# Kernel tuning notes

Measured on AMD Instinct MI355X. Metric: run time of the kernel, lower is better.

The kernel has to match this reference:

```python
import jax, jax.numpy as jnp
import numpy as np

B, VS, VO = 16, 10475, 8192
K, PS, PO = 64, 1024, 2048


def setup_inputs() -> dict:
    key = jax.random.key(0)
    k1, k2, k3, k4, k5 = jax.random.split(key, 5)
    smplx_v = jax.random.normal(k1, (B, VS, 3), dtype=jnp.float32)
    object_v = jax.random.normal(k2, (B, VO, 3), dtype=jnp.float32)
    smpl_part_idx = jax.random.randint(k3, (K, PS), 0, VS, dtype=jnp.int64) if jax.config.jax_enable_x64 else jax.random.randint(k3, (K, PS), 0, VS, dtype=jnp.int32)
    obj_part_idx = jax.random.randint(k4, (K, PO), 0, VO, dtype=jnp.int32)
    batch_idx = jax.random.randint(k5, (K,), 0, B, dtype=jnp.int32)
    return {
        'smplx_v': smplx_v,
        'object_v': object_v,
        'smpl_part_idx': smpl_part_idx,
        'obj_part_idx': obj_part_idx,
        'batch_idx': batch_idx,
    }


def reference(smplx_v, object_v, smpl_part_idx, obj_part_idx, batch_idx):
    # Batched gather of per-pair contact vertex subsets.
    sc = smplx_v[batch_idx[:, None], smpl_part_idx]   # [K, PS, 3]
    oc = object_v[batch_idx[:, None], obj_part_idx]   # [K, PO, 3]
    # Pairwise Euclidean distances [K, PS, PO] (torch.norm of differences).
    diff = sc[:, :, None, :] - oc[:, None, :, :]
    d = jnp.sqrt(jnp.sum(diff * diff, axis=-1))
    # One-directional chamfer: min over object verts, mean over smpl verts,
    # then mean over all contact pairs (torch.stack(...).mean()).
    loss = jnp.mean(jnp.mean(jnp.min(d, axis=-1), axis=-1))
    return loss
```

## Files before the change

### kernel.cpp

```cpp
#include <hip/hip_runtime.h>
#include <float.h>
#include <math.h>

constexpr int B  = 16;
constexpr int VS = 10475;
constexpr int VO = 8192;
constexpr int K  = 64;
constexpr int PS = 1024;
constexpr int PO = 2048;

constexpr int BLK  = 1024;
constexpr int QPB  = 256;
constexpr int GRID = K * (PS / QPB);
constexpr int NG   = 16;
constexpr int JPG  = PO / NG;
constexpr int QL   = 4;

typedef float v2f __attribute__((ext_vector_type(2)));
typedef float v3f __attribute__((ext_vector_type(3)));
typedef float v4f __attribute__((ext_vector_type(4)));


__global__ __launch_bounds__(BLK)
void cl_onepass(const float* __restrict__ smplx_v,
                const float* __restrict__ object_v,
                const int*   __restrict__ spi,
                const int*   __restrict__ opi,
                const int*   __restrict__ bidx,
                float*       __restrict__ partial)
{
    __shared__ v4f    so[PO];
    __shared__ float4 qld[QPB];
    __shared__ float  red[NG][QPB];
    __shared__ float  wsum[NG];

    const int bk  = blockIdx.x;
    const int tid = threadIdx.x;
    const int k   = bk >> 2;
    const int ic  = bk & 3;
    const int b   = bidx[k];

    const float* __restrict__ ov = object_v + (size_t)b * VO * 3;
    #pragma unroll
    for (int r = 0; r < PO / BLK; ++r) {
        const int j  = r * BLK + tid;
        const int oj = opi[k * PO + j];
        const v3f p  = *(const v3f*)(ov + 3 * (size_t)oj);
        so[j] = (v4f){p.x, p.y, p.z, 0.5f * (p.x * p.x + p.y * p.y + p.z * p.z)};
    }
    if (tid < QPB) {
        const int i  = ic * QPB + tid;
        const int si = spi[k * PS + i];
        const v3f s  = *(const v3f*)(smplx_v + 3 * ((size_t)b * VS + si));
        qld[tid] = make_float4(s.x, s.y, s.z, s.x * s.x + s.y * s.y + s.z * s.z);
    }
    __syncthreads();

    const int g    = tid >> 6;
    const int lane = tid & 63;
    const int qb   = lane * QL;

    v2f nsx[2], nsy[2], nsz[2], mint[2];
    #pragma unroll
    for (int p = 0; p < 2; ++p) {
        const float4 qa = qld[qb + 2 * p];
        const float4 qc = qld[qb + 2 * p + 1];
        nsx[p] = (v2f){-qa.x, -qc.x};
        nsy[p] = (v2f){-qa.y, -qc.y};
        nsz[p] = (v2f){-qa.z, -qc.z};
        mint[p] = (v2f){FLT_MAX, FLT_MAX};
    }

    const v4f* __restrict__ sog = &so[g * JPG];
    #pragma unroll 8
    for (int j = 0; j < JPG; ++j) {
        const v4f o = sog[j];
        const v2f oxy = __builtin_shufflevector(o, o, 0, 1);
        const v2f ozw = __builtin_shufflevector(o, o, 2, 3);
        #pragma unroll
        for (int p = 0; p < 2; ++p) {
            v2f t;
            asm("v_pk_fma_f32 %0, %1, %2, %3 op_sel:[0,0,1] op_sel_hi:[0,1,1]"
                : "=v"(t) : "v"(oxy), "v"(nsx[p]), "v"(ozw));
            asm("v_pk_fma_f32 %0, %1, %2, %0 op_sel:[1,0,0] op_sel_hi:[1,1,1]"
                : "+v"(t) : "v"(oxy), "v"(nsy[p]));
            asm("v_pk_fma_f32 %0, %1, %2, %0 op_sel:[0,0,0] op_sel_hi:[0,1,1]"
                : "+v"(t) : "v"(ozw), "v"(nsz[p]));
            mint[p].x = fminf(mint[p].x, t.x);
            mint[p].y = fminf(mint[p].y, t.y);
        }
    }

    #pragma unroll
    for (int p = 0; p < 2; ++p) {
        red[g][qb + 2 * p]     = mint[p].x;
        red[g][qb + 2 * p + 1] = mint[p].y;
    }
    __syncthreads();

    float d = 0.0f;
    if (tid < QPB) {
        float mq = red[0][tid];
        #pragma unroll
        for (int g2 = 1; g2 < NG; ++g2) mq = fminf(mq, red[g2][tid]);
        const float s2q = qld[tid].w;
        d = sqrtf(fmaxf(fmaf(2.0f, mq, s2q), 0.0f));
    }
    #pragma unroll
    for (int off = 32; off > 0; off >>= 1)
        d += __shfl_down(d, off, 64);
    if (lane == 0) wsum[g] = d;
    __syncthreads();
    if (tid < 64) {
        float v = (tid < NG) ? wsum[tid] : 0.0f;
        #pragma unroll
        for (int off = 8; off > 0; off >>= 1)
            v += __shfl_down(v, off, 64);
        if (tid == 0) partial[bk] = v;
    }
}


__global__ __launch_bounds__(64)
void cl_final(const float* __restrict__ partial, float* __restrict__ out)
{
    const int t = threadIdx.x;
    const float4 a = ((const float4*)partial)[t];
    float v = (a.x + a.y) + (a.z + a.w);
    #pragma unroll
    for (int off = 32; off > 0; off >>= 1)
        v += __shfl_down(v, off, 64);
    if (t == 0) out[0] = v * (1.0f / (float)(K * PS));
}


extern "C" void kernel_launch(void* const* d_in, const int* in_sizes, int n_in,
                              void* d_out, int out_size, void* d_ws, size_t ws_size,
                              hipStream_t stream)
{
    const float* smplx_v       = (const float*)d_in[0];
    const float* object_v      = (const float*)d_in[1];
    const int*   smpl_part_idx = (const int*)d_in[2];
    const int*   obj_part_idx  = (const int*)d_in[3];
    const int*   batch_idx     = (const int*)d_in[4];
    float*       out           = (float*)d_out;

    float* partial = (float*)d_ws;

    cl_onepass<<<GRID, BLK, 0, stream>>>(
        smplx_v, object_v, smpl_part_idx, obj_part_idx, batch_idx, partial);
    cl_final<<<1, 64, 0, stream>>>(partial, out);
}
```

Measured before the change: 19.16 us.

## Split object staging into two halves and overlap second gather with compute

The object-vertex staging is split into two shared buffers. The first half is gathered before the barrier. The second half's indexed global loads are issued after the barrier and held in registers while the first half is being computed, then written to shared memory behind a second barrier. This aims to hide the dependent gather latency behind the distance/min loop. In exchange it adds an extra barrier and more live registers per thread.

```diff
diff --git a/kernel.cpp b/kernel.cpp
--- a/kernel.cpp
+++ b/kernel.cpp
@@ -13,7 +13,8 @@
 constexpr int QPB  = 256;
 constexpr int GRID = K * (PS / QPB);
 constexpr int NG   = 16;
-constexpr int JPG  = PO / NG;
+constexpr int HALF = PO / 2;
+constexpr int JPH  = HALF / NG;
 constexpr int QL   = 4;
 
 typedef float v2f __attribute__((ext_vector_type(2)));
@@ -29,7 +30,8 @@
                 const int*   __restrict__ bidx,
                 float*       __restrict__ partial)
 {
-    __shared__ v4f    so[PO];
+    __shared__ v4f    soA[HALF];
+    __shared__ v4f    soB[HALF];
     __shared__ float4 qld[QPB];
     __shared__ float  red[NG][QPB];
     __shared__ float  wsum[NG];
@@ -40,21 +42,29 @@
     const int ic  = bk & 3;
     const int b   = bidx[k];
 
-    const float* __restrict__ ov = object_v + (size_t)b * VO * 3;
-    #pragma unroll
-    for (int r = 0; r < PO / BLK; ++r) {
-        const int j  = r * BLK + tid;
-        const int oj = opi[k * PO + j];
+    const float* __restrict__ ov   = object_v + (size_t)b * VO * 3;
+    const int*   __restrict__ opik = opi + k * PO;
+
+    {
+        const int oj = opik[tid];
         const v3f p  = *(const v3f*)(ov + 3 * (size_t)oj);
-        so[j] = (v4f){p.x, p.y, p.z, 0.5f * (p.x * p.x + p.y * p.y + p.z * p.z)};
+        soA[tid] = (v4f){p.x, p.y, p.z,
+                         0.5f * (p.x * p.x + p.y * p.y + p.z * p.z)};
     }
     if (tid < QPB) {
         const int i  = ic * QPB + tid;
         const int si = spi[k * PS + i];
         const v3f s  = *(const v3f*)(smplx_v + 3 * ((size_t)b * VS + si));
-        qld[tid] = make_float4(s.x, s.y, s.z, s.x * s.x + s.y * s.y + s.z * s.z);
+        qld[tid] = make_float4(s.x, s.y, s.z,
+                               s.x * s.x + s.y * s.y + s.z * s.z);
     }
     __syncthreads();
+
+    v3f p1;
+    {
+        const int oj = opik[HALF + tid];
+        p1 = *(const v3f*)(ov + 3 * (size_t)oj);
+    }
 
     const int g    = tid >> 6;
     const int lane = tid & 63;
@@ -71,25 +81,37 @@
         mint[p] = (v2f){FLT_MAX, FLT_MAX};
     }
 
-    const v4f* __restrict__ sog = &so[g * JPG];
-    #pragma unroll 8
-    for (int j = 0; j < JPG; ++j) {
-        const v4f o = sog[j];
-        const v2f oxy = __builtin_shufflevector(o, o, 0, 1);
-        const v2f ozw = __builtin_shufflevector(o, o, 2, 3);
-        #pragma unroll
-        for (int p = 0; p < 2; ++p) {
-            v2f t;
-            asm("v_pk_fma_f32 %0, %1, %2, %3 op_sel:[0,0,1] op_sel_hi:[0,1,1]"
-                : "=v"(t) : "v"(oxy), "v"(nsx[p]), "v"(ozw));
-            asm("v_pk_fma_f32 %0, %1, %2, %0 op_sel:[1,0,0] op_sel_hi:[1,1,1]"
-                : "+v"(t) : "v"(oxy), "v"(nsy[p]));
-            asm("v_pk_fma_f32 %0, %1, %2, %0 op_sel:[0,0,0] op_sel_hi:[0,1,1]"
-                : "+v"(t) : "v"(ozw), "v"(nsz[p]));
-            mint[p].x = fminf(mint[p].x, t.x);
-            mint[p].y = fminf(mint[p].y, t.y);
-        }
+    #define CL_BODY(SOH)                                                      \
+    {                                                                         \
+        const v4f* __restrict__ sog = &(SOH)[g * JPH];                        \
+        _Pragma("unroll 8")                                                   \
+        for (int j = 0; j < JPH; ++j) {                                       \
+            const v4f o = sog[j];                                             \
+            const v2f oxy = __builtin_shufflevector(o, o, 0, 1);              \
+            const v2f ozw = __builtin_shufflevector(o, o, 2, 3);              \
+            _Pragma("unroll")                                                 \
+            for (int p = 0; p < 2; ++p) {                                     \
+                v2f t;                                                        \
+                asm("v_pk_fma_f32 %0, %1, %2, %3 op_sel:[0,0,1] op_sel_hi:[0,1,1]" \
+                    : "=v"(t) : "v"(oxy), "v"(nsx[p]), "v"(ozw));             \
+                asm("v_pk_fma_f32 %0, %1, %2, %0 op_sel:[1,0,0] op_sel_hi:[1,1,1]" \
+                    : "+v"(t) : "v"(oxy), "v"(nsy[p]));                       \
+                asm("v_pk_fma_f32 %0, %1, %2, %0 op_sel:[0,0,0] op_sel_hi:[0,1,1]" \
+                    : "+v"(t) : "v"(ozw), "v"(nsz[p]));                       \
+                mint[p].x = fminf(mint[p].x, t.x);                            \
+                mint[p].y = fminf(mint[p].y, t.y);                            \
+            }                                                                 \
+        }                                                                     \
     }
+
+    CL_BODY(soA)
+
+    soB[tid] = (v4f){p1.x, p1.y, p1.z,
+                     0.5f * (p1.x * p1.x + p1.y * p1.y + p1.z * p1.z)};
+    __syncthreads();
+
+    CL_BODY(soB)
+    #undef CL_BODY
 
     #pragma unroll
     for (int p = 0; p < 2; ++p) {
```

Result: no change. 19.01 us (-0.8%).

## Compute chamfer distance dot products with fp16 MFMA using hi/lo split

Applied to the files above, without the earlier changes.

Replaces the packed-FP32 FMA inner loop with 16x16x32 fp16 MFMA instructions. Each wave handles 16 query points against all 2048 object points. Query coordinates are split into fp16 hi and lo parts, and the object norm term is also split in two, to keep accuracy close to fp32 while using matrix cores. Only lanes 0-15 feed real B data; the other lanes point at a zero pad. This wastes most of the K dimension and removes the cross-wave LDS min reduction in favour of shuffles. The object coordinates are rounded to fp16 with no lo correction, so accuracy against the fp32 reference is at risk.

```diff
diff --git a/kernel.cpp b/kernel.cpp
--- a/kernel.cpp
+++ b/kernel.cpp
@@ -12,13 +12,20 @@
 constexpr int BLK  = 1024;
 constexpr int QPB  = 256;
 constexpr int GRID = K * (PS / QPB);
-constexpr int NG   = 16;
-constexpr int JPG  = PO / NG;
-constexpr int QL   = 4;
+constexpr int NW   = 16;
+constexpr int NT   = PO / 16;
 
-typedef float v2f __attribute__((ext_vector_type(2)));
-typedef float v3f __attribute__((ext_vector_type(3)));
-typedef float v4f __attribute__((ext_vector_type(4)));
+typedef float  v3f  __attribute__((ext_vector_type(3)));
+typedef float  f32x4 __attribute__((ext_vector_type(4)));
+typedef _Float16 half8 __attribute__((ext_vector_type(8)));
+typedef unsigned int u32;
+typedef u32 v4u  __attribute__((ext_vector_type(4)));
+
+__device__ __forceinline__ u32 pkh(_Float16 lo, _Float16 hi) {
+    const unsigned short l = __builtin_bit_cast(unsigned short, lo);
+    const unsigned short h = __builtin_bit_cast(unsigned short, hi);
+    return ((u32)h << 16) | (u32)l;
+}
 
 
 __global__ __launch_bounds__(BLK)
@@ -29,16 +36,16 @@
                 const int*   __restrict__ bidx,
                 float*       __restrict__ partial)
 {
-    __shared__ v4f    so[PO];
-    __shared__ float4 qld[QPB];
-    __shared__ float  red[NG][QPB];
-    __shared__ float  wsum[NG];
+    __shared__ u32   so[(PO + 16) * 4];
+    __shared__ float wsum[NW];
 
-    const int bk  = blockIdx.x;
-    const int tid = threadIdx.x;
-    const int k   = bk >> 2;
-    const int ic  = bk & 3;
-    const int b   = bidx[k];
+    const int bk   = blockIdx.x;
+    const int tid  = threadIdx.x;
+    const int k    = bk >> 2;
+    const int ic   = bk & 3;
+    const int b    = bidx[k];
+    const int wave = tid >> 6;
+    const int lane = tid & 63;
 
     const float* __restrict__ ov = object_v + (size_t)b * VO * 3;
     #pragma unroll
@@ -46,73 +53,77 @@
         const int j  = r * BLK + tid;
         const int oj = opi[k * PO + j];
         const v3f p  = *(const v3f*)(ov + 3 * (size_t)oj);
-        so[j] = (v4f){p.x, p.y, p.z, 0.5f * (p.x * p.x + p.y * p.y + p.z * p.z)};
+        const _Float16 hx = (_Float16)p.x, hy = (_Float16)p.y, hz = (_Float16)p.z;
+        const float fx = (float)hx, fy = (float)hy, fz = (float)hz;
+        const float w2 = 0.5f * (fx * fx + fy * fy + fz * fz);
+        const _Float16 w2h = (_Float16)w2;
+        const _Float16 w2l = (_Float16)(w2 - (float)w2h);
+        const u32 d0 = pkh(hx, hy);
+        *(v4u*)&so[j * 4] = (v4u){d0, pkh(hz, w2h), d0, pkh(hz, w2l)};
     }
-    if (tid < QPB) {
-        const int i  = ic * QPB + tid;
+    if (tid < 64) so[PO * 4 + tid] = 0;
+
+    half8 afrag = (half8)(_Float16)0;
+    float s2 = 0.0f;
+    if (lane < 16) {
+        const int i  = ic * QPB + wave * 16 + lane;
         const int si = spi[k * PS + i];
         const v3f s  = *(const v3f*)(smplx_v + 3 * ((size_t)b * VS + si));
-        qld[tid] = make_float4(s.x, s.y, s.z, s.x * s.x + s.y * s.y + s.z * s.z);
+        s2 = s.x * s.x + s.y * s.y + s.z * s.z;
+        const _Float16 shx = (_Float16)s.x, shy = (_Float16)s.y, shz = (_Float16)s.z;
+        const _Float16 slx = (_Float16)(s.x - (float)shx);
+        const _Float16 sly = (_Float16)(s.y - (float)shy);
+        const _Float16 slz = (_Float16)(s.z - (float)shz);
+        const _Float16 n1  = (_Float16)(-1.0f);
+        afrag = (half8){shx, shy, shz, n1, slx, sly, slz, n1};
     }
     __syncthreads();
 
-    const int g    = tid >> 6;
-    const int lane = tid & 63;
-    const int qb   = lane * QL;
+    const u32* bp = (lane < 16) ? &so[lane * 4]
+                                : &so[PO * 4 + (lane & 15) * 4];
+    const int  inc = (lane < 16) ? 64 : 0;
 
-    v2f nsx[2], nsy[2], nsz[2], mint[2];
-    #pragma unroll
-    for (int p = 0; p < 2; ++p) {
-        const float4 qa = qld[qb + 2 * p];
-        const float4 qc = qld[qb + 2 * p + 1];
-        nsx[p] = (v2f){-qa.x, -qc.x};
-        nsy[p] = (v2f){-qa.y, -qc.y};
-        nsz[p] = (v2f){-qa.z, -qc.z};
-        mint[p] = (v2f){FLT_MAX, FLT_MAX};
-    }
-
-    const v4f* __restrict__ sog = &so[g * JPG];
+    f32x4 mint = (f32x4){FLT_MAX, FLT_MAX, FLT_MAX, FLT_MAX};
     #pragma unroll 8
-    for (int j = 0; j < JPG; ++j) {
-        const v4f o = sog[j];
-        const v2f oxy = __builtin_shufflevector(o, o, 0, 1);
-        const v2f ozw = __builtin_shufflevector(o, o, 2, 3);
-        #pragma unroll
-        for (int p = 0; p < 2; ++p) {
-            v2f t;
-            asm("v_pk_fma_f32 %0, %1, %2, %3 op_sel:[0,0,1] op_sel_hi:[0,1,1]"
-                : "=v"(t) : "v"(oxy), "v"(nsx[p]), "v"(ozw));
-            asm("v_pk_fma_f32 %0, %1, %2, %0 op_sel:[1,0,0] op_sel_hi:[1,1,1]"
-                : "+v"(t) : "v"(oxy), "v"(nsy[p]));
-            asm("v_pk_fma_f32 %0, %1, %2, %0 op_sel:[0,0,0] op_sel_hi:[0,1,1]"
-                : "+v"(t) : "v"(ozw), "v"(nsz[p]));
-            mint[p].x = fminf(mint[p].x, t.x);
-            mint[p].y = fminf(mint[p].y, t.y);
-        }
+    for (int t = 0; t < NT; ++t) {
+        const half8 bfrag = *(const half8*)bp;
+        const f32x4 d = __builtin_amdgcn_mfma_f32_16x16x32_f16(
+            afrag, bfrag, (f32x4){0.f, 0.f, 0.f, 0.f}, 0, 0, 0);
+        mint.x = fminf(mint.x, -d.x);
+        mint.y = fminf(mint.y, -d.y);
+        mint.z = fminf(mint.z, -d.z);
+        mint.w = fminf(mint.w, -d.w);
+        bp += inc;
     }
 
     #pragma unroll
-    for (int p = 0; p < 2; ++p) {
-        red[g][qb + 2 * p]     = mint[p].x;
-        red[g][qb + 2 * p + 1] = mint[p].y;
+    for (int m = 1; m <= 8; m <<= 1) {
+        mint.x = fminf(mint.x, __shfl_xor(mint.x, m, 64));
+        mint.y = fminf(mint.y, __shfl_xor(mint.y, m, 64));
+        mint.z = fminf(mint.z, __shfl_xor(mint.z, m, 64));
+        mint.w = fminf(mint.w, __shfl_xor(mint.w, m, 64));
     }
+
+    const int src = (lane >> 2) << 4;
+    const float t0 = __shfl(mint.x, src, 64);
+    const float t1 = __shfl(mint.y, src, 64);
+    const float t2 = __shfl(mint.z, src, 64);
+    const float t3 = __shfl(mint.w, src, 64);
+    const int rsel = lane & 3;
+    const float tmy = (rsel == 0) ? t0 : (rsel == 1) ? t1 : (rsel == 2) ? t2 : t3;
+
+    float d = 0.0f;
+    if (lane < 16)
+        d = sqrtf(fmaxf(fmaf(2.0f, tmy, s2), 0.0f));
+
+    #pragma unroll
+    for (int m = 1; m <= 8; m <<= 1)
+        d += __shfl_xor(d, m, 64);
+    if (lane == 0) wsum[wave] = d;
     __syncthreads();
 
-    float d = 0.0f;
-    if (tid < QPB) {
-        float mq = red[0][tid];
-        #pragma unroll
-        for (int g2 = 1; g2 < NG; ++g2) mq = fminf(mq, red[g2][tid]);
-        const float s2q = qld[tid].w;
-        d = sqrtf(fmaxf(fmaf(2.0f, mq, s2q), 0.0f));
-    }
-    #pragma unroll
-    for (int off = 32; off > 0; off >>= 1)
-        d += __shfl_down(d, off, 64);
-    if (lane == 0) wsum[g] = d;
-    __syncthreads();
     if (tid < 64) {
-        float v = (tid < NG) ? wsum[tid] : 0.0f;
+        float v = (tid < NW) ? wsum[tid] : 0.0f;
         #pragma unroll
         for (int off = 8; off > 0; off >>= 1)
             v += __shfl_down(v, off, 64);
```

Result: faster. 16.51 us (-13.8%).
